# Kernel tuning notes

Hardware: AMD Instinct MI355X
Metric: run time of the kernel (lower is better)

Reference implementation:

```python
import jax, jax.numpy as jnp
import numpy as np

N = 50000      # nodes
E = 800000     # edges (avg degree 16)
F_IN = 128
# (d_in, d_out) for the 9 GCNConv layers with width=256, n_layers=3
DIMS = [(128, 128), (128, 192), (192, 256), (256, 256), (256, 256), (256, 256), (256, 192), (192, 128), (128, 1)]
# ReLU after every conv except loop conv i==n_layers-2 (conv idx 4) and the final conv
RELU = [True, True, True, True, False, True, True, True, False]


def setup_inputs() -> dict:
    key = jax.random.key(0)
    ks = jax.random.split(key, 2 + 2 * len(DIMS))
    inp = {
        "x": jax.random.normal(ks[0], (N, F_IN), dtype=jnp.float32),
        "edge_index": jax.random.randint(ks[1], (2, E), 0, N, dtype=jnp.int64),
    }
    for i, (din, dout) in enumerate(DIMS):
        # Glorot-ish init for weights, small random bias (GCNConv has bias=True)
        inp[f"W{i}"] = jax.random.normal(ks[2 + 2 * i], (din, dout), dtype=jnp.float32) / np.float32(np.sqrt(din))
        inp[f"b{i}"] = jax.random.normal(ks[3 + 2 * i], (dout,), dtype=jnp.float32) * 0.01
    return inp


def _gcn_stack(x, src_f, dst_f, norm, Ws, bs):
    h = x
    for i in range(len(Ws)):
        h = h @ Ws[i]                                  # [N, dout] dense transform first (dout <= din mostly)
        msg = h[src_f] * norm[:, None]                 # gather + edge-normalize  [E+N, dout]
        h = jax.ops.segment_sum(msg, dst_f, num_segments=N) + bs[i]
        if RELU[i]:
            h = jax.nn.relu(h)
        # Dropout layers are identity in eval/inference mode.
    return h


def reference(x, edge_index,
              W0, b0, W1, b1, W2, b2, W3, b3, W4, b4, W5, b5, W6, b6, W7, b7, W8, b8):
    src, dst = edge_index[0], edge_index[1]
    loop = jnp.arange(N, dtype=src.dtype)
    # GCNConv default: add self loops, symmetric normalization D^{-1/2}(A+I)D^{-1/2}
    src_f = jnp.concatenate([src, loop])
    dst_f = jnp.concatenate([dst, loop])
    deg = jax.ops.segment_sum(jnp.ones(E + N, dtype=x.dtype), dst_f, num_segments=N)
    dinv = jax.lax.rsqrt(jnp.maximum(deg, 1.0))        # deg >= 1 thanks to self loops
    norm = dinv[src_f] * dinv[dst_f]                   # per-edge coefficient [E+N]
    Ws = [W0, W1, W2, W3, W4, W5, W6, W7, W8]
    bs = [b0, b1, b2, b3, b4, b5, b6, b7, b8]
    return _gcn_stack(x, src_f, dst_f, norm, Ws, bs)   # [N, 1]
```

## Files before the change

kernel.cpp:

```cpp
#include <hip/hip_runtime.h>


#define TPB 256

using bf16x8 = __attribute__((ext_vector_type(8))) __bf16;
using f32x4  = __attribute__((ext_vector_type(4))) float;
using f32x2  = __attribute__((ext_vector_type(2))) float;

__device__ __forceinline__ unsigned bf16rne(float x) {
    unsigned u = __float_as_uint(x);
    return (u + 0x7fffu + ((u >> 16) & 1u)) >> 16;
}

__device__ __forceinline__ f32x2 bl2(unsigned u) {
    return (f32x2){__uint_as_float(u << 16), __uint_as_float(u & 0xffff0000u)};
}

__device__ __forceinline__ void stage16(const unsigned short* g, unsigned short* l) {
#if __has_builtin(__builtin_amdgcn_global_load_lds)
    __builtin_amdgcn_global_load_lds((const __attribute__((address_space(1))) void*)g,
                                     (__attribute__((address_space(3))) void*)l, 16, 0, 0);
#else
    *(uint4*)((char*)l + (threadIdx.x & 63) * 16) = *(const uint4*)g;
#endif
}


__global__ void zinit_kernel(int* cnt, int* fill, int n) {
    int i = blockIdx.x * blockDim.x + threadIdx.x;
    if (i < n) { cnt[i] = 0; fill[i] = 0; }
}

__global__ void count_kernel(const int* __restrict__ dst, int* __restrict__ cnt, int E) {
    int e = blockIdx.x * blockDim.x + threadIdx.x;
    if (e < E) atomicAdd(&cnt[dst[e]], 1);
}


__global__ void blockhist_kernel(const int* __restrict__ cnt, int* __restrict__ localRank,
                                 int* __restrict__ hb, float* __restrict__ dinv,
                                 int n, int nb) {
    __shared__ int h[64];
    int t = threadIdx.x;
    if (t < 64) h[t] = 0;
    __syncthreads();
    int i = blockIdx.x * TPB + t;
    if (i < n) {
        int c = cnt[i];
        dinv[i] = rsqrtf((float)(c + 1));
        int d = c; if (d > 63) d = 63;
        localRank[i] = atomicAdd(&h[d], 1);
    }
    __syncthreads();
    if (t < 64) hb[t * nb + blockIdx.x] = h[t];
}

__global__ __launch_bounds__(256) void sortscan_kernel(int* __restrict__ hb, int nb) {
    __shared__ int sh[64 * 256];
    __shared__ int tot[64], base[64];
    int t = threadIdx.x;
    int total = 64 * nb;
    for (int i = t; i < total; i += 256) sh[i] = hb[i];
    __syncthreads();
    if (t < 64) {
        int run = 0;
        for (int b = 0; b < nb; b++) {
            int v = sh[t * nb + b];
            sh[t * nb + b] = run;
            run += v;
        }
        tot[t] = run;
    }
    __syncthreads();
    if (t == 0) {
        int acc = 0;
        for (int b = 0; b < 64; b++) { base[b] = acc; acc += tot[b]; }
    }
    __syncthreads();
    for (int i = t; i < total; i += 256) hb[i] = sh[i] + base[i / nb];
}

__global__ void scatter2_kernel(const int* __restrict__ cnt,
                                const int* __restrict__ localRank, const int* __restrict__ hb,
                                int* __restrict__ perm, int* __restrict__ pcnt,
                                int* __restrict__ iperm, int n, int nb) {
    int i = blockIdx.x * TPB + threadIdx.x;
    if (i >= n) return;
    int c = cnt[i];
    int d = c; if (d > 63) d = 63;
    int pos = hb[d * nb + blockIdx.x] + localRank[i];
    perm[pos] = i;
    pcnt[pos] = c;
    iperm[i] = pos;
}

__global__ void scan1_kernel(const int* __restrict__ pcnt, int* __restrict__ prowp2,
                             int* __restrict__ bsums, int n) {
    __shared__ int sh[TPB];
    int t = threadIdx.x;
    int i = blockIdx.x * TPB + t;
    int v = (i < n) ? (pcnt[i] + 1) : 0;
    sh[t] = v;
    __syncthreads();
    for (int off = 1; off < TPB; off <<= 1) {
        int x = (t >= off) ? sh[t - off] : 0;
        __syncthreads();
        sh[t] += x;
        __syncthreads();
    }
    if (i < n) prowp2[i] = sh[t] - v;
    if (t == TPB - 1) bsums[blockIdx.x] = sh[t];
}

__global__ void scan2_kernel(int* __restrict__ bsums, int nb) {
    __shared__ int sh[TPB];
    int t = threadIdx.x;
    int v = (t < nb) ? bsums[t] : 0;
    sh[t] = v;
    __syncthreads();
    for (int off = 1; off < TPB; off <<= 1) {
        int x = (t >= off) ? sh[t - off] : 0;
        __syncthreads();
        sh[t] += x;
        __syncthreads();
    }
    if (t < nb) bsums[t] = sh[t] - v;
}

__global__ void scan3_kernel(int* __restrict__ rowp, const int* __restrict__ bsums, int n) {
    int i = blockIdx.x * TPB + threadIdx.x;
    if (i < n) rowp[i] += bsums[blockIdx.x];
}

__global__ void fillself_kernel(const int* __restrict__ src, const int* __restrict__ dst,
                                const float* __restrict__ dinv,
                                const int* __restrict__ iperm, const int* __restrict__ prowp2,
                                int* __restrict__ fill, const int* __restrict__ cnt,
                                unsigned* __restrict__ edges2, int E, int n) {
    int id = blockIdx.x * blockDim.x + threadIdx.x;
    if (id < E) {
        int s = src[id], d = dst[id];
        int pos = prowp2[iperm[d]] + atomicAdd(&fill[d], 1);
        edges2[pos] = (unsigned)s | (bf16rne(dinv[s] * dinv[d]) << 16);
    } else if (id < E + n) {
        int i = id - E;
        float dv = dinv[i];
        edges2[prowp2[iperm[i]] + cnt[i]] = (unsigned)i | (bf16rne(dv * dv) << 16);
    }
}


struct WPtrs { const float* p[8]; };

__global__ void wt_all_kernel(WPtrs wp, unsigned short* __restrict__ Wts) {
    const int cum[9] = {0, 16384, 40960, 90112, 155648, 221184, 286720, 335872, 360448};
    const int Ns[8] = {128, 192, 256, 256, 256, 256, 192, 128};
    const int Ks[8] = {128, 128, 192, 256, 256, 256, 256, 192};
    int id = blockIdx.x * blockDim.x + threadIdx.x;
    if (id >= 360448) return;
    int L = 0;
#pragma unroll
    for (int t = 1; t < 8; t++) if (id >= cum[t]) L = t;
    int lid = id - cum[L];
    int N = Ns[L], K = Ks[L];
    int k = lid / N, n = lid - k * N;
    Wts[cum[L] + n * K + k] = (unsigned short)bf16rne(wp.p[L][lid]);
}

__global__ void cvt_bf16_kernel(const float* __restrict__ in, unsigned short* __restrict__ out,
                                int n4) {
    int i = blockIdx.x * blockDim.x + threadIdx.x;
    if (i >= n4) return;
    float4 v = ((const float4*)in)[i];
    uint2 o;
    o.x = bf16rne(v.x) | (bf16rne(v.y) << 16);
    o.y = bf16rne(v.z) | (bf16rne(v.w) << 16);
    ((uint2*)out)[i] = o;
}


__global__ __launch_bounds__(256) void gemm_mfma_kernel(
    const unsigned short* __restrict__ A, const unsigned short* __restrict__ Wt,
    const float* __restrict__ bias, unsigned short* __restrict__ C,
    int M, int K, int Nc, int doBias, int doRelu, int outChunked) {
    __shared__ unsigned short Qb[128 * 64];
    __shared__ unsigned short Pb[128 * 64];
    int tid = threadIdx.x;
    int l = tid & 63, w = tid >> 6;
    int node0 = blockIdx.x * 128, feat0 = blockIdx.y * 128;

    f32x4 acc[4][4];
#pragma unroll
    for (int i = 0; i < 4; i++)
#pragma unroll
        for (int j = 0; j < 4; j++) acc[i][j] = (f32x4){0.f, 0.f, 0.f, 0.f};

    const unsigned short* gQ[4];
    const unsigned short* gP[4];
    unsigned short* lQ[4];
    unsigned short* lP[4];
#pragma unroll
    for (int h = 0; h < 4; h++) {
        int slot = tid + h * 256;
        int r = slot >> 3, q = slot & 7;
        int qg = q ^ (r & 7);
        int nd = node0 + r; if (nd > M - 1) nd = M - 1;
        int ft = feat0 + r; if (ft > Nc - 1) ft = Nc - 1;
        gQ[h] = A + (size_t)nd * K + qg * 8;
        gP[h] = Wt + (size_t)ft * K + qg * 8;
        lQ[h] = Qb + (size_t)(w * 64 + h * 256) * 8;
        lP[h] = Pb + (size_t)(w * 64 + h * 256) * 8;
    }

    int q4 = l >> 4, m16 = l & 15;
    int featHalf = w & 1, nodeHalf = w >> 1;
    int rP0 = featHalf * 64 + m16;
    int rQ0 = nodeHalf * 64 + m16;
    int sw = m16 & 7;

    for (int k0 = 0; k0 < K; k0 += 64) {
        __syncthreads();
#pragma unroll
        for (int h = 0; h < 4; h++) {
            stage16(gQ[h] + k0, lQ[h]);
            stage16(gP[h] + k0, lP[h]);
        }
        __syncthreads();
#pragma unroll
        for (int ko = 0; ko < 2; ko++) {
            bf16x8 pf[4], qf[4];
#pragma unroll
            for (int i = 0; i < 4; i++)
                pf[i] = *(const bf16x8*)(Pb + (rP0 + i * 16) * 64 + ((ko * 4 + q4) ^ sw) * 8);
#pragma unroll
            for (int j = 0; j < 4; j++)
                qf[j] = *(const bf16x8*)(Qb + (rQ0 + j * 16) * 64 + ((ko * 4 + q4) ^ sw) * 8);
#pragma unroll
            for (int i = 0; i < 4; i++)
#pragma unroll
                for (int j = 0; j < 4; j++)
                    acc[i][j] = __builtin_amdgcn_mfma_f32_16x16x32_bf16(pf[i], qf[j],
                                                                        acc[i][j], 0, 0, 0);
        }
    }

#pragma unroll
    for (int i = 0; i < 4; i++) {
        int gf0 = feat0 + featHalf * 64 + i * 16 + q4 * 4;
        if (gf0 >= Nc) continue;
        float4 bv = make_float4(0.f, 0.f, 0.f, 0.f);
        if (doBias) bv = *(const float4*)(bias + gf0);
        size_t cb = outChunked ? ((size_t)(gf0 >> 5) * ((size_t)M * 32) + (gf0 & 31))
                               : (size_t)gf0;
#pragma unroll
        for (int j = 0; j < 4; j++) {
            int gn = node0 + nodeHalf * 64 + j * 16 + m16;
            if (gn >= M) continue;
            f32x4 v = acc[i][j];
            float x0 = v[0] + bv.x, x1 = v[1] + bv.y;
            float x2 = v[2] + bv.z, x3 = v[3] + bv.w;
            if (doRelu) {
                x0 = fmaxf(x0, 0.f); x1 = fmaxf(x1, 0.f);
                x2 = fmaxf(x2, 0.f); x3 = fmaxf(x3, 0.f);
            }
            uint2 o;
            o.x = bf16rne(x0) | (bf16rne(x1) << 16);
            o.y = bf16rne(x2) | (bf16rne(x3) << 16);
            size_t off = outChunked ? (cb + (size_t)gn * 32) : (cb + (size_t)gn * Nc);
            *(uint2*)(C + off) = o;
        }
    }
}

__global__ void gemv128_bf16_kernel(const unsigned short* __restrict__ A,
                                    const float* __restrict__ w,
                                    float* __restrict__ out, int M) {
    int wid = (blockIdx.x * blockDim.x + threadIdx.x) >> 6;
    int lane = threadIdx.x & 63;
    if (wid >= M) return;
    const unsigned short* a = A + (size_t)wid * 128;
    float a0 = __uint_as_float((unsigned)a[lane] << 16);
    float a1 = __uint_as_float((unsigned)a[lane + 64] << 16);
    float s = a0 * w[lane] + a1 * w[lane + 64];
#pragma unroll
    for (int off = 32; off > 0; off >>= 1) s += __shfl_down(s, off);
    if (lane == 0) out[wid] = s;
}


__global__ __launch_bounds__(256) void agg_group_kernel(
    const uint4* __restrict__ in, const int* __restrict__ prowp2,
    const int* __restrict__ pcnt, const int* __restrict__ perm,
    const unsigned* __restrict__ edges2,
    const float* __restrict__ bias, uint4* __restrict__ out,
    int Q, int upx, int ngPerUnit, int NG, int n_nodes, int rowVec4,
    int doBias, int doRelu, int outChunked) {
    int xcd = blockIdx.x & 7;
    int slot = blockIdx.x >> 3;
    int u = slot / ngPerUnit;
    int ngIdx = slot - u * ngPerUnit;
    int unit = xcd * upx + u;
    int chunk = unit / Q;
    int q = unit - chunk * Q;
    int ng = ngIdx * Q + q;
    if (ng >= NG) return;
    ng = NG - 1 - ng;

    int wave = threadIdx.x >> 6;
    int lane = threadIdx.x & 63;
    int group = lane >> 2, fl = lane & 3;
    int gb = lane & ~3;
    int i = ng * 64 + wave * 16 + group;
    if (i >= n_nodes) return;

    const uint4* sf = in + (size_t)chunk * n_nodes * 4 + fl;
    int s0 = prowp2[i];
    int c = pcnt[i] + 1;
    int node = perm[i];
    const unsigned* ep = edges2 + s0;

    f32x2 acc[2][4];
#pragma unroll
    for (int k = 0; k < 2; k++)
#pragma unroll
        for (int m = 0; m < 4; m++) acc[k][m] = (f32x2){0.f, 0.f};

    unsigned ewA = (fl < c) ? ep[fl] : 0u;
    unsigned ewB = (4 + fl < c) ? ep[4 + fl] : 0u;
    unsigned eA[4]; uint4 pA[4];
#pragma unroll
    for (int j = 0; j < 4; j++) eA[j] = (unsigned)__shfl((int)ewA, gb + j);
#pragma unroll
    for (int j = 0; j < 4; j++) pA[j] = sf[(size_t)(eA[j] & 0xffffu) * 4];

    for (int base = 0; base < c; base += 8) {
        unsigned ewC = (base + 8 + fl < c) ? ep[base + 8 + fl] : 0u;
        unsigned eB[4]; uint4 pB[4];
#pragma unroll
        for (int j = 0; j < 4; j++) eB[j] = (unsigned)__shfl((int)ewB, gb + j);
#pragma unroll
        for (int j = 0; j < 4; j++) pB[j] = sf[(size_t)(eB[j] & 0xffffu) * 4];
#pragma unroll
        for (int j = 0; j < 4; j++) {
            float wgt = __uint_as_float(eA[j] & 0xffff0000u);
            f32x2 w2 = {wgt, wgt};
            int k = j & 1;
            acc[k][0] += w2 * bl2(pA[j].x);
            acc[k][1] += w2 * bl2(pA[j].y);
            acc[k][2] += w2 * bl2(pA[j].z);
            acc[k][3] += w2 * bl2(pA[j].w);
        }
        unsigned ewD = (base + 12 + fl < c) ? ep[base + 12 + fl] : 0u;
#pragma unroll
        for (int j = 0; j < 4; j++) eA[j] = (unsigned)__shfl((int)ewC, gb + j);
#pragma unroll
        for (int j = 0; j < 4; j++) pA[j] = sf[(size_t)(eA[j] & 0xffffu) * 4];
#pragma unroll
        for (int j = 0; j < 4; j++) {
            float wgt = __uint_as_float(eB[j] & 0xffff0000u);
            f32x2 w2 = {wgt, wgt};
            int k = j & 1;
            acc[k][0] += w2 * bl2(pB[j].x);
            acc[k][1] += w2 * bl2(pB[j].y);
            acc[k][2] += w2 * bl2(pB[j].z);
            acc[k][3] += w2 * bl2(pB[j].w);
        }
        ewB = ewD;
    }
    f32x2 s[4];
#pragma unroll
    for (int m = 0; m < 4; m++) s[m] = acc[0][m] + acc[1][m];

    if (doBias) {
        const float* bp = bias + chunk * 32 + fl * 8;
        float4 b0 = *(const float4*)bp;
        float4 b1 = *(const float4*)(bp + 4);
        s[0] += (f32x2){b0.x, b0.y};
        s[1] += (f32x2){b0.z, b0.w};
        s[2] += (f32x2){b1.x, b1.y};
        s[3] += (f32x2){b1.z, b1.w};
    }
    if (doRelu) {
#pragma unroll
        for (int m = 0; m < 4; m++) {
            s[m][0] = fmaxf(s[m][0], 0.f);
            s[m][1] = fmaxf(s[m][1], 0.f);
        }
    }
    uint4 o;
    o.x = bf16rne(s[0][0]) | (bf16rne(s[0][1]) << 16);
    o.y = bf16rne(s[1][0]) | (bf16rne(s[1][1]) << 16);
    o.z = bf16rne(s[2][0]) | (bf16rne(s[2][1]) << 16);
    o.w = bf16rne(s[3][0]) | (bf16rne(s[3][1]) << 16);
    size_t oi = outChunked ? ((size_t)chunk * n_nodes * 4 + (size_t)node * 4 + fl)
                           : ((size_t)node * rowVec4 + chunk * 4 + fl);
    out[oi] = o;
}

__global__ void agg1_kernel(const float* __restrict__ in, const int* __restrict__ prowp2,
                            const int* __restrict__ pcnt, const int* __restrict__ perm,
                            const unsigned* __restrict__ edges2,
                            const float* __restrict__ bias, float* __restrict__ out,
                            int n_nodes) {
    int n = blockIdx.x * blockDim.x + threadIdx.x;
    if (n >= n_nodes) return;
    float acc = 0.f;
    int s0 = prowp2[n];
    int c = pcnt[n] + 1;
    for (int j = 0; j < c; j++) {
        unsigned e = edges2[s0 + j];
        acc += __uint_as_float(e & 0xffff0000u) * in[e & 0xffffu];
    }
    acc += bias[0];
    out[perm[n]] = acc;
}


extern "C" void kernel_launch(void* const* d_in, const int* in_sizes, int n_in,
                              void* d_out, int out_size, void* d_ws, size_t ws_size,
                              hipStream_t stream) {
    const float* x = (const float*)d_in[0];
    const int* ei = (const int*)d_in[1];
    const int Nn = in_sizes[0] / 128;
    const int E = in_sizes[1] / 2;
    const int* src = ei;
    const int* dst = ei + E;

    char* ws = (char*)d_ws;
    size_t off = 0;
    auto alloc = [&](size_t bytes) -> char* {
        char* p = ws + off;
        off = (off + bytes + 255) & ~(size_t)255;
        return p;
    };
    int* cnt = (int*)alloc((size_t)Nn * 4);
    int* fill = (int*)alloc((size_t)Nn * 4);
    int* bsums = (int*)alloc(1024);
    float* dinv = (float*)alloc((size_t)Nn * 4);
    int* localRank = (int*)alloc((size_t)Nn * 4);
    int* hb = (int*)alloc((size_t)64 * 256 * 4);
    int* perm = (int*)alloc((size_t)Nn * 4);
    int* pcnt = (int*)alloc((size_t)Nn * 4);
    int* iperm = (int*)alloc((size_t)Nn * 4);
    int* prowp2 = (int*)alloc((size_t)Nn * 4);
    unsigned* edges2 = (unsigned*)alloc((size_t)(E + Nn + 64) * 4);
    unsigned short* T = (unsigned short*)alloc((size_t)Nn * 256 * 2);
    unsigned short* H = (unsigned short*)alloc((size_t)Nn * 256 * 2);
    unsigned short* Bx = (unsigned short*)alloc((size_t)Nn * 128 * 2);
    float* F = (float*)alloc((size_t)Nn * 4);
    unsigned short* Wts = (unsigned short*)alloc((size_t)400000 * 2);
    (void)ws_size;

    const int dims[9][2] = {{128,128},{128,192},{192,256},{256,256},{256,256},
                            {256,256},{256,192},{192,128},{128,1}};
    unsigned short* Wt[8];
    {
        size_t o = 0;
        for (int i = 0; i < 8; i++) { Wt[i] = Wts + o; o += (size_t)dims[i][0] * dims[i][1]; }
    }

    int nbN = (Nn + TPB - 1) / TPB;
    int nbE = (E + TPB - 1) / TPB;
    int nbEN = (E + Nn + TPB - 1) / TPB;

    zinit_kernel<<<nbN, TPB, 0, stream>>>(cnt, fill, Nn);
    count_kernel<<<nbE, TPB, 0, stream>>>(dst, cnt, E);
    blockhist_kernel<<<nbN, TPB, 0, stream>>>(cnt, localRank, hb, dinv, Nn, nbN);
    sortscan_kernel<<<1, 256, 0, stream>>>(hb, nbN);
    scatter2_kernel<<<nbN, TPB, 0, stream>>>(cnt, localRank, hb, perm, pcnt, iperm,
                                             Nn, nbN);
    scan1_kernel<<<nbN, TPB, 0, stream>>>(pcnt, prowp2, bsums, Nn);
    scan2_kernel<<<1, TPB, 0, stream>>>(bsums, nbN);
    scan3_kernel<<<nbN, TPB, 0, stream>>>(prowp2, bsums, Nn);
    fillself_kernel<<<nbEN, TPB, 0, stream>>>(src, dst, dinv, iperm, prowp2, fill, cnt,
                                              edges2, E, Nn);

    WPtrs wp;
    for (int i = 0; i < 8; i++) wp.p[i] = (const float*)d_in[2 + 2 * i];
    wt_all_kernel<<<(360448 + TPB - 1) / TPB, TPB, 0, stream>>>(wp, Wts);
    cvt_bf16_kernel<<<(Nn * 32 + TPB - 1) / TPB, TPB, 0, stream>>>(x, Bx, Nn * 32);

    auto gemm = [&](const unsigned short* A, int i, unsigned short* C, int K, int Nc,
                    int doBias, int doRelu, int outChunked) {
        const float* b = (const float*)d_in[3 + 2 * i];
        dim3 grid((Nn + 127) / 128, (Nc + 127) / 128);
        gemm_mfma_kernel<<<grid, 256, 0, stream>>>(A, Wt[i], b, C, Nn, K, Nc,
                                                   doBias, doRelu, outChunked);
    };
    int NG = (Nn + 63) / 64;
    auto agg = [&](const unsigned short* inb, unsigned short* outb, int w, int i,
                   int doBias, int doRelu, int outChunked) {
        int nch = w / 32;
        int Q = (nch == 8) ? 1 : (nch == 6) ? 4 : 2;
        int upx = nch * Q / 8;
        int ngPerUnit = (NG + Q - 1) / Q;
        int blocksPerXcd = upx * ngPerUnit;
        const float* b = (const float*)d_in[3 + 2 * i];
        agg_group_kernel<<<blocksPerXcd * 8, 256, 0, stream>>>(
            (const uint4*)inb, prowp2, pcnt, perm, edges2, b, (uint4*)outb,
            Q, upx, ngPerUnit, NG, Nn, w / 8, doBias, doRelu, outChunked);
    };

    gemm(Bx, 0, T, 128, 128, 0, 0, 1);
    agg(T, H, 128, 0, 1, 1, 1);
    agg(H, T, 128, 1, 0, 0, 0);
    gemm(T, 1, H, 128, 192, 1, 1, 1);
    agg(H, T, 192, 2, 0, 0, 0);
    gemm(T, 2, H, 192, 256, 1, 1, 0);
    gemm(H, 3, T, 256, 256, 0, 0, 1);
    agg(T, H, 256, 3, 1, 1, 0);
    gemm(H, 4, T, 256, 256, 0, 0, 1);
    agg(T, H, 256, 4, 1, 0, 0);
    gemm(H, 5, T, 256, 256, 0, 0, 1);
    agg(T, H, 256, 5, 1, 1, 0);
    gemm(H, 6, T, 256, 192, 0, 0, 1);
    agg(T, H, 192, 6, 1, 1, 0);
    gemm(H, 7, T, 192, 128, 0, 0, 1);
    agg(T, H, 128, 7, 1, 1, 0);
    gemv128_bf16_kernel<<<(Nn + 3) / 4, 256, 0, stream>>>(H, (const float*)d_in[2 + 16],
                                                          F, Nn);
    agg1_kernel<<<nbN, TPB, 0, stream>>>(F, prowp2, pcnt, perm, edges2,
                                         (const float*)d_in[3 + 16], (float*)d_out, Nn);
}
```

Before: 653.2 us.

## Widen aggregation feature chunks to 64 and precompute edge ranks in CSR build

The chunked feature layout goes from 32 to 64 bf16 columns per chunk, so each node row is handled by 8 lanes of 16 bytes (128 bytes) per gather instead of 4 lanes (64 bytes). Each wave now covers 8 nodes instead of 16, and the grid/Q mapping across XCDs is retuned to match. The CSR fill records each edge's atomic rank during the count pass and precomputes per-node row offsets, removing the second atomic pass and the double indirection. Wider gathers should use memory transactions better, at the cost of fewer nodes per wave, an extra rank array of E ints and one more small kernel.

```diff
diff --git a/kernel.cpp b/kernel.cpp
--- a/kernel.cpp
+++ b/kernel.cpp
@@ -26,14 +26,15 @@
 }
 
 
-__global__ void zinit_kernel(int* cnt, int* fill, int n) {
+__global__ void zinit_kernel(int* cnt, int n) {
     int i = blockIdx.x * blockDim.x + threadIdx.x;
-    if (i < n) { cnt[i] = 0; fill[i] = 0; }
-}
-
-__global__ void count_kernel(const int* __restrict__ dst, int* __restrict__ cnt, int E) {
+    if (i < n) cnt[i] = 0;
+}
+
+__global__ void count_kernel(const int* __restrict__ dst, int* __restrict__ cnt,
+                             int* __restrict__ rank, int E) {
     int e = blockIdx.x * blockDim.x + threadIdx.x;
-    if (e < E) atomicAdd(&cnt[dst[e]], 1);
+    if (e < E) rank[e] = atomicAdd(&cnt[dst[e]], 1);
 }
 
 
@@ -132,20 +133,27 @@
     if (i < n) rowp[i] += bsums[blockIdx.x];
 }
 
+__global__ void rowo_kernel(const int* __restrict__ iperm, const int* __restrict__ prowp2,
+                            int* __restrict__ rowo, int n) {
+    int i = blockIdx.x * TPB + threadIdx.x;
+    if (i < n) rowo[i] = prowp2[iperm[i]];
+}
+
 __global__ void fillself_kernel(const int* __restrict__ src, const int* __restrict__ dst,
+                                const int* __restrict__ rank,
                                 const float* __restrict__ dinv,
-                                const int* __restrict__ iperm, const int* __restrict__ prowp2,
-                                int* __restrict__ fill, const int* __restrict__ cnt,
+                                const int* __restrict__ rowo,
+                                const int* __restrict__ cnt,
                                 unsigned* __restrict__ edges2, int E, int n) {
     int id = blockIdx.x * blockDim.x + threadIdx.x;
     if (id < E) {
         int s = src[id], d = dst[id];
-        int pos = prowp2[iperm[d]] + atomicAdd(&fill[d], 1);
+        int pos = rowo[d] + rank[id];
         edges2[pos] = (unsigned)s | (bf16rne(dinv[s] * dinv[d]) << 16);
     } else if (id < E + n) {
         int i = id - E;
         float dv = dinv[i];
-        edges2[prowp2[iperm[i]] + cnt[i]] = (unsigned)i | (bf16rne(dv * dv) << 16);
+        edges2[rowo[i] + cnt[i]] = (unsigned)i | (bf16rne(dv * dv) << 16);
     }
 }
 
@@ -250,7 +258,7 @@
         if (gf0 >= Nc) continue;
         float4 bv = make_float4(0.f, 0.f, 0.f, 0.f);
         if (doBias) bv = *(const float4*)(bias + gf0);
-        size_t cb = outChunked ? ((size_t)(gf0 >> 5) * ((size_t)M * 32) + (gf0 & 31))
+        size_t cb = outChunked ? ((size_t)(gf0 >> 6) * ((size_t)M * 64) + (gf0 & 63))
                                : (size_t)gf0;
 #pragma unroll
         for (int j = 0; j < 4; j++) {
@@ -266,7 +274,7 @@
             uint2 o;
             o.x = bf16rne(x0) | (bf16rne(x1) << 16);
             o.y = bf16rne(x2) | (bf16rne(x3) << 16);
-            size_t off = outChunked ? (cb + (size_t)gn * 32) : (cb + (size_t)gn * Nc);
+            size_t off = outChunked ? (cb + (size_t)gn * 64) : (cb + (size_t)gn * Nc);
             *(uint2*)(C + off) = o;
         }
     }
@@ -308,12 +316,12 @@
 
     int wave = threadIdx.x >> 6;
     int lane = threadIdx.x & 63;
-    int group = lane >> 2, fl = lane & 3;
-    int gb = lane & ~3;
-    int i = ng * 64 + wave * 16 + group;
+    int group = lane >> 3, fl = lane & 7;
+    int gb = lane & ~7;
+    int i = ng * 32 + wave * 8 + group;
     if (i >= n_nodes) return;
 
-    const uint4* sf = in + (size_t)chunk * n_nodes * 4 + fl;
+    const uint4* sf = in + (size_t)chunk * n_nodes * 8 + fl;
     int s0 = prowp2[i];
     int c = pcnt[i] + 1;
     int node = perm[i];
@@ -325,21 +333,20 @@
 #pragma unroll
         for (int m = 0; m < 4; m++) acc[k][m] = (f32x2){0.f, 0.f};
 
-    unsigned ewA = (fl < c) ? ep[fl] : 0u;
-    unsigned ewB = (4 + fl < c) ? ep[4 + fl] : 0u;
+    unsigned ew = (fl < c) ? ep[fl] : 0u;
     unsigned eA[4]; uint4 pA[4];
 #pragma unroll
-    for (int j = 0; j < 4; j++) eA[j] = (unsigned)__shfl((int)ewA, gb + j);
-#pragma unroll
-    for (int j = 0; j < 4; j++) pA[j] = sf[(size_t)(eA[j] & 0xffffu) * 4];
+    for (int j = 0; j < 4; j++) eA[j] = (unsigned)__shfl((int)ew, gb + j);
+#pragma unroll
+    for (int j = 0; j < 4; j++) pA[j] = sf[(size_t)(eA[j] & 0xffffu) * 8];
 
     for (int base = 0; base < c; base += 8) {
-        unsigned ewC = (base + 8 + fl < c) ? ep[base + 8 + fl] : 0u;
+        unsigned ewn = (base + 8 + fl < c) ? ep[base + 8 + fl] : 0u;
         unsigned eB[4]; uint4 pB[4];
 #pragma unroll
-        for (int j = 0; j < 4; j++) eB[j] = (unsigned)__shfl((int)ewB, gb + j);
-#pragma unroll
-        for (int j = 0; j < 4; j++) pB[j] = sf[(size_t)(eB[j] & 0xffffu) * 4];
+        for (int j = 0; j < 4; j++) eB[j] = (unsigned)__shfl((int)ew, gb + 4 + j);
+#pragma unroll
+        for (int j = 0; j < 4; j++) pB[j] = sf[(size_t)(eB[j] & 0xffffu) * 8];
 #pragma unroll
         for (int j = 0; j < 4; j++) {
             float wgt = __uint_as_float(eA[j] & 0xffff0000u);
@@ -350,11 +357,10 @@
             acc[k][2] += w2 * bl2(pA[j].z);
             acc[k][3] += w2 * bl2(pA[j].w);
         }
-        unsigned ewD = (base + 12 + fl < c) ? ep[base + 12 + fl] : 0u;
-#pragma unroll
-        for (int j = 0; j < 4; j++) eA[j] = (unsigned)__shfl((int)ewC, gb + j);
-#pragma unroll
-        for (int j = 0; j < 4; j++) pA[j] = sf[(size_t)(eA[j] & 0xffffu) * 4];
+#pragma unroll
+        for (int j = 0; j < 4; j++) eA[j] = (unsigned)__shfl((int)ewn, gb + j);
+#pragma unroll
+        for (int j = 0; j < 4; j++) pA[j] = sf[(size_t)(eA[j] & 0xffffu) * 8];
 #pragma unroll
         for (int j = 0; j < 4; j++) {
             float wgt = __uint_as_float(eB[j] & 0xffff0000u);
@@ -365,14 +371,14 @@
             acc[k][2] += w2 * bl2(pB[j].z);
             acc[k][3] += w2 * bl2(pB[j].w);
         }
-        ewB = ewD;
+        ew = ewn;
     }
     f32x2 s[4];
 #pragma unroll
     for (int m = 0; m < 4; m++) s[m] = acc[0][m] + acc[1][m];
 
     if (doBias) {
-        const float* bp = bias + chunk * 32 + fl * 8;
+        const float* bp = bias + chunk * 64 + fl * 8;
         float4 b0 = *(const float4*)bp;
         float4 b1 = *(const float4*)(bp + 4);
         s[0] += (f32x2){b0.x, b0.y};
@@ -392,8 +398,8 @@
     o.y = bf16rne(s[1][0]) | (bf16rne(s[1][1]) << 16);
     o.z = bf16rne(s[2][0]) | (bf16rne(s[2][1]) << 16);
     o.w = bf16rne(s[3][0]) | (bf16rne(s[3][1]) << 16);
-    size_t oi = outChunked ? ((size_t)chunk * n_nodes * 4 + (size_t)node * 4 + fl)
-                           : ((size_t)node * rowVec4 + chunk * 4 + fl);
+    size_t oi = outChunked ? ((size_t)chunk * n_nodes * 8 + (size_t)node * 8 + fl)
+                           : ((size_t)node * rowVec4 + chunk * 8 + fl);
     out[oi] = o;
 }
 
@@ -434,7 +440,7 @@
         return p;
     };
     int* cnt = (int*)alloc((size_t)Nn * 4);
-    int* fill = (int*)alloc((size_t)Nn * 4);
+    int* rank = (int*)alloc((size_t)E * 4);
     int* bsums = (int*)alloc(1024);
     float* dinv = (float*)alloc((size_t)Nn * 4);
     int* localRank = (int*)alloc((size_t)Nn * 4);
@@ -443,6 +449,7 @@
     int* pcnt = (int*)alloc((size_t)Nn * 4);
     int* iperm = (int*)alloc((size_t)Nn * 4);
     int* prowp2 = (int*)alloc((size_t)Nn * 4);
+    int* rowo = (int*)alloc((size_t)Nn * 4);
     unsigned* edges2 = (unsigned*)alloc((size_t)(E + Nn + 64) * 4);
     unsigned short* T = (unsigned short*)alloc((size_t)Nn * 256 * 2);
     unsigned short* H = (unsigned short*)alloc((size_t)Nn * 256 * 2);
@@ -463,8 +470,8 @@
     int nbE = (E + TPB - 1) / TPB;
     int nbEN = (E + Nn + TPB - 1) / TPB;
 
-    zinit_kernel<<<nbN, TPB, 0, stream>>>(cnt, fill, Nn);
-    count_kernel<<<nbE, TPB, 0, stream>>>(dst, cnt, E);
+    zinit_kernel<<<nbN, TPB, 0, stream>>>(cnt, Nn);
+    count_kernel<<<nbE, TPB, 0, stream>>>(dst, cnt, rank, E);
     blockhist_kernel<<<nbN, TPB, 0, stream>>>(cnt, localRank, hb, dinv, Nn, nbN);
     sortscan_kernel<<<1, 256, 0, stream>>>(hb, nbN);
     scatter2_kernel<<<nbN, TPB, 0, stream>>>(cnt, localRank, hb, perm, pcnt, iperm,
@@ -472,7 +479,8 @@
     scan1_kernel<<<nbN, TPB, 0, stream>>>(pcnt, prowp2, bsums, Nn);
     scan2_kernel<<<1, TPB, 0, stream>>>(bsums, nbN);
     scan3_kernel<<<nbN, TPB, 0, stream>>>(prowp2, bsums, Nn);
-    fillself_kernel<<<nbEN, TPB, 0, stream>>>(src, dst, dinv, iperm, prowp2, fill, cnt,
+    rowo_kernel<<<nbN, TPB, 0, stream>>>(iperm, prowp2, rowo, Nn);
+    fillself_kernel<<<nbEN, TPB, 0, stream>>>(src, dst, rank, dinv, rowo, cnt,
                                               edges2, E, Nn);
 
     WPtrs wp;
@@ -487,11 +495,11 @@
         gemm_mfma_kernel<<<grid, 256, 0, stream>>>(A, Wt[i], b, C, Nn, K, Nc,
                                                    doBias, doRelu, outChunked);
     };
-    int NG = (Nn + 63) / 64;
+    int NG = (Nn + 31) / 32;
     auto agg = [&](const unsigned short* inb, unsigned short* outb, int w, int i,
                    int doBias, int doRelu, int outChunked) {
-        int nch = w / 32;
-        int Q = (nch == 8) ? 1 : (nch == 6) ? 4 : 2;
+        int nch = w / 64;
+        int Q = (nch == 4) ? 2 : (nch == 3) ? 8 : 4;
         int upx = nch * Q / 8;
         int ngPerUnit = (NG + Q - 1) / Q;
         int blocksPerXcd = upx * ngPerUnit;
```

After: 581.7 us. -10.9%, faster.
